# Optimization experiments

Measured on AMD Instinct MI355X. Metric: run time of the kernel, lower is better.

The kernel has to match this reference:

```python
import jax, jax.numpy as jnp
import numpy as np

B, T, C, H, N = 4, 4096, 2048, 32, 64
DMIX, DDEC = 32, 64
N_LAYER, LAYER_ID = 24, 12
GN_EPS = 1e-5 * 8.0 ** 2  # eps = 1e-5 * head_size_divisor**2


def setup_inputs() -> dict:
    key = jax.random.key(0)
    ks = jax.random.split(key, 24)
    r01 = LAYER_ID / (N_LAYER - 1)
    r1a0 = 1.0 - LAYER_ID / N_LAYER
    ddd = (np.arange(C, dtype=np.float32) / C).reshape(1, 1, C)
    maa = lambda p: jnp.asarray(1.0 - ddd ** p, dtype=jnp.float32)
    # decay speed schedule (canonical RWKV6, over channel dim)
    n = np.arange(C, dtype=np.float32)
    decay = (-6.0 + 5.0 * (n / (C - 1)) ** (0.7 + 1.3 * r01)).reshape(1, 1, C)
    # time_faaaa zigzag schedule
    m = np.arange(C, dtype=np.float32)
    zig = ((m + 1) % 3 - 1) * 0.1
    faaaa = (r01 * (1 - m / (C - 1)) + zig).reshape(H, N)
    s = 1.0 / np.sqrt(C)
    return {
        "x": jax.random.normal(ks[0], (B, T, C), jnp.float32),
        "shift_state": jax.random.normal(ks[1], (B, C), jnp.float32),
        "wkv_state": jnp.zeros((B, H, N, N), jnp.float32),
        "time_maa_x": maa(r1a0),
        "time_maa_w": maa(r1a0),
        "time_maa_k": maa(r1a0),
        "time_maa_v": jnp.asarray(1.0 - (ddd ** r1a0 + 0.3 * r01), jnp.float32),
        "time_maa_r": maa(0.5 * r1a0),
        "time_maa_g": maa(0.5 * r1a0),
        "time_maa_w1": jax.random.normal(ks[2], (C, 5 * DMIX), jnp.float32) * 0.01,
        "time_maa_w2": jax.random.uniform(ks[3], (5, DMIX, C), jnp.float32, -0.01, 0.01),
        "time_decay": jnp.asarray(decay, jnp.float32),
        "time_decay_w1": jax.random.normal(ks[4], (C, DDEC), jnp.float32) * 0.01,
        "time_decay_w2": jax.random.uniform(ks[5], (DDEC, C), jnp.float32, -0.01, 0.01),
        "time_faaaa": jnp.asarray(faaaa, jnp.float32),
        "Wr": jax.random.normal(ks[6], (C, C), jnp.float32) * s,
        "Wk": jax.random.normal(ks[7], (C, C), jnp.float32) * s,
        "Wv": jax.random.normal(ks[8], (C, C), jnp.float32) * s,
        "Wg": jax.random.normal(ks[9], (C, C), jnp.float32) * s,
        "Wo": jax.random.normal(ks[10], (C, C), jnp.float32) * s,
        "gn_weight": jnp.ones((C,), jnp.float32),
        "gn_bias": jnp.zeros((C,), jnp.float32),
    }


def reference(x, shift_state, wkv_state, time_maa_x, time_maa_w, time_maa_k,
              time_maa_v, time_maa_r, time_maa_g, time_maa_w1, time_maa_w2,
              time_decay, time_decay_w1, time_decay_w2, time_faaaa,
              Wr, Wk, Wv, Wg, Wo, gn_weight, gn_bias):
    b, t, c = x.shape
    # token shift: previous token (seeded by shift_state) minus current
    xx = jnp.concatenate([shift_state[:, None, :], x[:, :-1]], axis=1) - x
    lx = x[:, -1]
    # LoRA token-shift mixing
    xxx = x + xx * time_maa_x
    t5 = jnp.tanh(xxx @ time_maa_w1).reshape(b, t, 5, DMIX)
    mixes = jnp.einsum('btfd,fdc->fbtc', t5, time_maa_w2)
    mw, mk, mv, mr, mg = mixes
    xw = x + xx * (time_maa_w + mw)
    xk = x + xx * (time_maa_k + mk)
    xv = x + xx * (time_maa_v + mv)
    xr = x + xx * (time_maa_r + mr)
    xg = x + xx * (time_maa_g + mg)
    r = xr @ Wr
    k = xk @ Wk
    v = xv @ Wv
    g = jax.nn.silu(xg @ Wg)
    # data-dependent decay via LoRA; wkv6 uses log-decay -exp(w)
    w = time_decay + jnp.tanh(xw @ time_decay_w1) @ time_decay_w2
    glog = -jnp.exp(w)  # [b,t,c]
    to_heads = lambda z: z.reshape(b, t, H, N).transpose(1, 0, 2, 3)  # [t,b,h,n]
    rh, kh, vh, gh = to_heads(r), to_heads(k), to_heads(v), to_heads(glog)
    u = time_faaaa  # [H,N]

    def step(S, inp):
        r_t, k_t, v_t, g_t = inp  # each [b,h,n]
        kv = jnp.einsum('bhk,bhv->bhkv', k_t, v_t)
        o_t = jnp.einsum('bhk,bhkv->bhv', r_t, S + u[None, :, :, None] * kv)
        S = jnp.exp(g_t)[..., None] * S + kv
        return S, o_t

    state, o = jax.lax.scan(step, wkv_state, (rh, kh, vh, gh))
    o = o.transpose(1, 0, 2, 3).reshape(b, t, c)  # [b,t,c]
    # GroupNorm with H groups over channel dim
    og = o.reshape(b, t, H, N)
    mu = og.mean(-1, keepdims=True)
    var = og.var(-1, keepdims=True)
    on = (og - mu) * jax.lax.rsqrt(var + GN_EPS)
    on = on * gn_weight.reshape(H, N) + gn_bias.reshape(H, N)
    out = (on.reshape(b, t, c) * g) @ Wo
    return out, lx, state
```

## Files before the change

### kernel.cpp

```cpp
#include <hip/hip_runtime.h>
#include <hip/hip_bf16.h>
#include <stdint.h>

#define DEV __device__ __forceinline__

typedef __bf16 bf16x8 __attribute__((ext_vector_type(8)));
typedef float f32x4 __attribute__((ext_vector_type(4)));
typedef unsigned short u16x8 __attribute__((ext_vector_type(8)));

constexpr int kB = 4, kT = 4096, kC = 2048, kH = 32, kN = 64;
constexpr int kM = kB * kT;
constexpr int SEGN = 8, TSEG = kT / SEGN, CHN = TSEG / 64;

DEV float bfu2f(unsigned short u) {
  union { uint32_t i; float f; } x; x.i = ((uint32_t)u) << 16; return x.f;
}
DEV unsigned short f2bfu(float f) {
  union { float f; uint32_t i; } x; x.f = f;
  uint32_t r = x.i + 0x7FFFu + ((x.i >> 16) & 1u);
  return (unsigned short)(r >> 16);
}

DEV void gld16(const void* g, void* l) {
  __builtin_amdgcn_global_load_lds(
      (const __attribute__((address_space(1))) void*)g,
      (__attribute__((address_space(3))) void*)l, 16, 0, 0);
}

DEV int swzb(int row, int byteoff) { return (row << 7) + (byteoff ^ ((row & 7) << 4)); }

__global__ __launch_bounds__(256) void trans_bf16(
    const float* __restrict__ in, unsigned short* __restrict__ out, int R, int Cn) {
  __shared__ __attribute__((aligned(16))) unsigned short tile[64][65];
  const int t = threadIdx.x;
  const int r0 = blockIdx.y * 64, c0 = blockIdx.x * 64;
  const int lr = t >> 6, lc = t & 63;
#pragma unroll
  for (int i = 0; i < 16; i++) {
    int rr = lr + i * 4;
    int gr = r0 + rr, gc = c0 + lc;
    if (gr < R && gc < Cn) tile[rr][lc] = f2bfu(in[(size_t)gr * Cn + gc]);
  }
  __syncthreads();
#pragma unroll
  for (int i = 0; i < 16; i++) {
    int cc = lr + i * 4;
    int gc = c0 + cc, gr = r0 + lc;
    if (gc < Cn && gr < R) out[(size_t)gc * R + gr] = tile[lc][cc];
  }
}

__global__ __launch_bounds__(256) void prep_x2(
    const float* __restrict__ x, const float* __restrict__ shift,
    const float* __restrict__ maax,
    unsigned short* __restrict__ xxx, float* __restrict__ lx) {
  size_t i4 = ((size_t)blockIdx.x * 256 + threadIdx.x) * 4;
  int c = (int)(i4 & (kC - 1));
  size_t bt = i4 >> 11;
  int tt = (int)(bt & (kT - 1));
  int b = (int)(bt >> 12);
  float4 xv = *(const float4*)(x + i4);
  float4 pv = (tt == 0) ? *(const float4*)(shift + (size_t)b * kC + c)
                        : *(const float4*)(x + i4 - kC);
  float4 mx = *(const float4*)(maax + c);
  ushort4 o4;
  o4.x = f2bfu(xv.x + (pv.x - xv.x) * mx.x);
  o4.y = f2bfu(xv.y + (pv.y - xv.y) * mx.y);
  o4.z = f2bfu(xv.z + (pv.z - xv.z) * mx.z);
  o4.w = f2bfu(xv.w + (pv.w - xv.w) * mx.w);
  *(ushort4*)(xxx + i4) = o4;
  if (tt == kT - 1) *(float4*)(lx + (size_t)b * kC + c) = xv;
}

enum { E_F32 = 0, E_BF16 = 1, E_TANH = 2, E_SILU = 3, E_DECAY = 4 };

template <int BM, int BN, int EPI>
__global__ __launch_bounds__(256) void gemm_k(
    const unsigned short* __restrict__ A, const unsigned short* __restrict__ Bt,
    void* __restrict__ Cout, const float* __restrict__ aux, int M, int N, int K) {
  constexpr int WGM = (BM == 128 && BN == 128) ? 2 : (BM == 64 ? 2 : 4);
  constexpr int WGN = 4 / WGM;
  constexpr int WM = BM / WGM, WN = BN / WGN;
  constexpr int WR = WM / 16, WC = WN / 16;
  __shared__ __attribute__((aligned(16))) unsigned short As[BM * 32];
  __shared__ __attribute__((aligned(16))) unsigned short Bs[BN * 32];
  const int t = threadIdx.x, wid = t >> 6, l = t & 63;
  const int m0 = blockIdx.x * BM, n0 = blockIdx.y * BN;
  const int wm0 = (wid / WGN) * WM, wn0 = (wid % WGN) * WN;
  f32x4 acc[WR][WC];
#pragma unroll
  for (int i = 0; i < WR; i++)
#pragma unroll
    for (int j = 0; j < WC; j++) acc[i][j] = f32x4{0.f, 0.f, 0.f, 0.f};

  const int rowS = t >> 2, cbS = (t & 3) * 16;
  const char* Ab = (const char*)A;
  const char* Bb = (const char*)Bt;
  const int aoff = (wm0 + (l & 15)) * 32 + (l >> 4) * 8;
  const int boff = (wn0 + (l & 15)) * 32 + (l >> 4) * 8;

  for (int kt = 0; kt < K; kt += 32) {
#pragma unroll
    for (int ia = 0; ia < BM / 64; ia++)
      gld16(Ab + ((size_t)(m0 + ia * 64 + rowS) * K + kt) * 2 + cbS,
            (char*)As + ia * 4096 + wid * 1024);
    if constexpr (BN >= 64) {
#pragma unroll
      for (int ib = 0; ib < BN / 64; ib++)
        gld16(Bb + ((size_t)(n0 + ib * 64 + rowS) * K + kt) * 2 + cbS,
              (char*)Bs + ib * 4096 + wid * 1024);
    } else {
      if (t < BN * 4)
        gld16(Bb + ((size_t)(n0 + rowS) * K + kt) * 2 + cbS,
              (char*)Bs + wid * 1024);
    }
    __syncthreads();
    bf16x8 af[WR], bfv[WC];
#pragma unroll
    for (int mi = 0; mi < WR; mi++) af[mi] = *(const bf16x8*)(&As[aoff + mi * 512]);
#pragma unroll
    for (int ni = 0; ni < WC; ni++) bfv[ni] = *(const bf16x8*)(&Bs[boff + ni * 512]);
#pragma unroll
    for (int mi = 0; mi < WR; mi++)
#pragma unroll
      for (int ni = 0; ni < WC; ni++)
        acc[mi][ni] = __builtin_amdgcn_mfma_f32_16x16x32_bf16(af[mi], bfv[ni], acc[mi][ni], 0, 0, 0);
    __syncthreads();
  }

#pragma unroll
  for (int mi = 0; mi < WR; mi++) {
#pragma unroll
    for (int ni = 0; ni < WC; ni++) {
      int row = m0 + wm0 + mi * 16 + (l >> 4) * 4;
      int col = n0 + wn0 + ni * 16 + (l & 15);
#pragma unroll
      for (int j = 0; j < 4; j++) {
        float v = acc[mi][ni][j];
        size_t idx = (size_t)(row + j) * N + col;
        if constexpr (EPI == E_F32) ((float*)Cout)[idx] = v;
        else if constexpr (EPI == E_BF16) ((unsigned short*)Cout)[idx] = f2bfu(v);
        else if constexpr (EPI == E_TANH) ((unsigned short*)Cout)[idx] = f2bfu(tanhf(v));
        else if constexpr (EPI == E_SILU) ((unsigned short*)Cout)[idx] = f2bfu(v / (1.f + expf(-v)));
        else if constexpr (EPI == E_DECAY) {
          float w = v + aux[col];
          ((float*)Cout)[idx] = expf(-expf(w));
        }
      }
    }
  }
}

template <int EPI>
__global__ __launch_bounds__(512, 2) void gemm256_k(
    const unsigned short* __restrict__ A, const unsigned short* __restrict__ Bt,
    void* __restrict__ Cout, int M, int N, int K) {
  extern __shared__ __attribute__((aligned(16))) char lds[];
  const int tid = threadIdx.x, wid = tid >> 6, l = tid & 63;

  const int mtiles = M >> 8, ntiles = N >> 8;
  const int slab = mtiles >> 3;
  const int xcd = blockIdx.x & 7, loc = blockIdx.x >> 3;
  const int m0 = (xcd * slab + loc / ntiles) * 256;
  const int n0 = (loc % ntiles) * 256;

  const int wm = (wid >> 2) * 128, wn = (wid & 3) * 64;

  const int srow = tid >> 3;
  const int scb = (tid & 7) * 16;
  const char* pa[4]; const char* pb[4];
#pragma unroll
  for (int i = 0; i < 4; i++) {
    int row = i * 64 + srow;
    int cb = scb ^ ((row & 7) << 4);
    pa[i] = (const char*)A + (size_t)(m0 + row) * K * 2 + cb;
    pb[i] = (const char*)Bt + (size_t)(n0 + row) * K * 2 + cb;
  }

  int aof[2][2][8], bof[2][2][4];
#pragma unroll
  for (int bu = 0; bu < 2; bu++)
#pragma unroll
    for (int ks = 0; ks < 2; ks++) {
#pragma unroll
      for (int mi = 0; mi < 8; mi++)
        aof[bu][ks][mi] = bu * 65536 + swzb(wm + mi * 16 + (l & 15), ks * 64 + (l >> 4) * 16);
#pragma unroll
      for (int ni = 0; ni < 4; ni++)
        bof[bu][ks][ni] = bu * 65536 + 32768 + swzb(wn + ni * 16 + (l & 15), ks * 64 + (l >> 4) * 16);
    }

  f32x4 acc[8][4];
#pragma unroll
  for (int i = 0; i < 8; i++)
#pragma unroll
    for (int j = 0; j < 4; j++) acc[i][j] = f32x4{0.f, 0.f, 0.f, 0.f};

  auto STAGE = [&](int bu, int tb) {
#pragma unroll
    for (int i = 0; i < 4; i++) {
      gld16(pa[i] + tb, lds + bu * 65536 + i * 8192 + wid * 1024);
      gld16(pb[i] + tb, lds + bu * 65536 + 32768 + i * 8192 + wid * 1024);
    }
  };
  auto COMPUTE = [&](int bu) {
    __builtin_amdgcn_s_setprio(1);
#pragma unroll
    for (int ks = 0; ks < 2; ks++) {
      bf16x8 a[8];
#pragma unroll
      for (int mi = 0; mi < 8; mi++) a[mi] = *(const bf16x8*)(lds + aof[bu][ks][mi]);
#pragma unroll
      for (int ni = 0; ni < 4; ni++) {
        bf16x8 b = *(const bf16x8*)(lds + bof[bu][ks][ni]);
#pragma unroll
        for (int mi = 0; mi < 8; mi++)
          acc[mi][ni] = __builtin_amdgcn_mfma_f32_16x16x32_bf16(a[mi], b, acc[mi][ni], 0, 0, 0);
      }
    }
    __builtin_amdgcn_s_setprio(0);
  };

  const int KT = K >> 6;
  STAGE(0, 0);
  STAGE(1, 128);

  for (int t = 0; t + 3 < KT; t += 2) {
    asm volatile("s_waitcnt vmcnt(8)" ::: "memory");
    __builtin_amdgcn_s_barrier();
    __builtin_amdgcn_sched_barrier(0);
    COMPUTE(0);
    asm volatile("s_waitcnt lgkmcnt(0)" ::: "memory");
    __builtin_amdgcn_s_barrier();
    __builtin_amdgcn_sched_barrier(0);
    STAGE(0, (t + 2) * 128);

    asm volatile("s_waitcnt vmcnt(8)" ::: "memory");
    __builtin_amdgcn_s_barrier();
    __builtin_amdgcn_sched_barrier(0);
    COMPUTE(1);
    asm volatile("s_waitcnt lgkmcnt(0)" ::: "memory");
    __builtin_amdgcn_s_barrier();
    __builtin_amdgcn_sched_barrier(0);
    STAGE(1, (t + 3) * 128);
  }

  asm volatile("s_waitcnt vmcnt(8)" ::: "memory");
  __builtin_amdgcn_s_barrier();
  __builtin_amdgcn_sched_barrier(0);
  COMPUTE(0);
  asm volatile("s_waitcnt vmcnt(0)" ::: "memory");
  __builtin_amdgcn_s_barrier();
  __builtin_amdgcn_sched_barrier(0);
  COMPUTE(1);

#pragma unroll
  for (int mi = 0; mi < 8; mi++)
#pragma unroll
    for (int ni = 0; ni < 4; ni++) {
      int row = m0 + wm + mi * 16 + (l >> 4) * 4;
      int col = n0 + wn + ni * 16 + (l & 15);
#pragma unroll
      for (int j = 0; j < 4; j++) {
        float v = acc[mi][ni][j];
        size_t idx = (size_t)(row + j) * N + col;
        if constexpr (EPI == E_F32) ((float*)Cout)[idx] = v;
        else if constexpr (EPI == E_BF16) ((unsigned short*)Cout)[idx] = f2bfu(v);
        else if constexpr (EPI == E_SILU) ((unsigned short*)Cout)[idx] = f2bfu(v / (1.f + expf(-v)));
      }
    }
}

__global__ __launch_bounds__(256) void mix2f_k(
    const unsigned short* __restrict__ t5, const unsigned short* __restrict__ w2t,
    const float* __restrict__ x, const float* __restrict__ shift,
    const float* __restrict__ maa1, const float* __restrict__ maa2,
    unsigned short* __restrict__ xo1, unsigned short* __restrict__ xo2,
    int f1, int f2) {
  __shared__ __attribute__((aligned(16))) unsigned short As1[64 * 32];
  __shared__ __attribute__((aligned(16))) unsigned short Bs1[64 * 32];
  __shared__ __attribute__((aligned(16))) unsigned short As2[64 * 32];
  __shared__ __attribute__((aligned(16))) unsigned short Bs2[64 * 32];
  const int t = threadIdx.x, wid = t >> 6, l = t & 63;
  const int m0 = blockIdx.x * 64, n0 = blockIdx.y * 64;
  const int wm0 = (wid >> 1) * 32, wn0 = (wid & 1) * 32;
  const int rowS = t >> 2, cbS = (t & 3) * 16;
  const int aoff = (wm0 + (l & 15)) * 32 + (l >> 4) * 8;
  const int boff = (wn0 + (l & 15)) * 32 + (l >> 4) * 8;

  gld16((const char*)t5 + ((size_t)(m0 + rowS) * 160 + f1 * 32) * 2 + cbS, (char*)As1 + wid * 1024);
  gld16((const char*)w2t + ((size_t)(n0 + rowS) * 160 + f1 * 32) * 2 + cbS, (char*)Bs1 + wid * 1024);
  gld16((const char*)t5 + ((size_t)(m0 + rowS) * 160 + f2 * 32) * 2 + cbS, (char*)As2 + wid * 1024);
  gld16((const char*)w2t + ((size_t)(n0 + rowS) * 160 + f2 * 32) * 2 + cbS, (char*)Bs2 + wid * 1024);
  __syncthreads();
  bf16x8 a10 = *(const bf16x8*)(&As1[aoff]), a11 = *(const bf16x8*)(&As1[aoff + 512]);
  bf16x8 b10 = *(const bf16x8*)(&Bs1[boff]), b11 = *(const bf16x8*)(&Bs1[boff + 512]);
  bf16x8 a20 = *(const bf16x8*)(&As2[aoff]), a21 = *(const bf16x8*)(&As2[aoff + 512]);
  bf16x8 b20 = *(const bf16x8*)(&Bs2[boff]), b21 = *(const bf16x8*)(&Bs2[boff + 512]);
  f32x4 ac1[2][2], ac2[2][2];
#pragma unroll
  for (int i = 0; i < 2; i++)
#pragma unroll
    for (int j = 0; j < 2; j++) { ac1[i][j] = f32x4{0.f, 0.f, 0.f, 0.f}; ac2[i][j] = f32x4{0.f, 0.f, 0.f, 0.f}; }
  ac1[0][0] = __builtin_amdgcn_mfma_f32_16x16x32_bf16(a10, b10, ac1[0][0], 0, 0, 0);
  ac1[0][1] = __builtin_amdgcn_mfma_f32_16x16x32_bf16(a10, b11, ac1[0][1], 0, 0, 0);
  ac1[1][0] = __builtin_amdgcn_mfma_f32_16x16x32_bf16(a11, b10, ac1[1][0], 0, 0, 0);
  ac1[1][1] = __builtin_amdgcn_mfma_f32_16x16x32_bf16(a11, b11, ac1[1][1], 0, 0, 0);
  ac2[0][0] = __builtin_amdgcn_mfma_f32_16x16x32_bf16(a20, b20, ac2[0][0], 0, 0, 0);
  ac2[0][1] = __builtin_amdgcn_mfma_f32_16x16x32_bf16(a20, b21, ac2[0][1], 0, 0, 0);
  ac2[1][0] = __builtin_amdgcn_mfma_f32_16x16x32_bf16(a21, b20, ac2[1][0], 0, 0, 0);
  ac2[1][1] = __builtin_amdgcn_mfma_f32_16x16x32_bf16(a21, b21, ac2[1][1], 0, 0, 0);

#pragma unroll
  for (int mi = 0; mi < 2; mi++)
#pragma unroll
    for (int ni = 0; ni < 2; ni++) {
      int row = m0 + wm0 + mi * 16 + (l >> 4) * 4;
      int col = n0 + wn0 + ni * 16 + (l & 15);
      float mv1 = maa1[col], mv2 = maa2[col];
#pragma unroll
      for (int j = 0; j < 4; j++) {
        int rrow = row + j;
        int tt = rrow & (kT - 1);
        size_t idx = (size_t)rrow * kC + col;
        float xv = x[idx];
        float pv = (tt == 0) ? shift[(size_t)(rrow >> 12) * kC + col] : x[idx - kC];
        float d = pv - xv;
        xo1[idx] = f2bfu(xv + d * (mv1 + ac1[mi][ni][j]));
        xo2[idx] = f2bfu(xv + d * (mv2 + ac2[mi][ni][j]));
      }
    }
}

__global__ __launch_bounds__(256) void mixf_k(
    const unsigned short* __restrict__ t5, const unsigned short* __restrict__ w2t,
    const float* __restrict__ x, const float* __restrict__ shift,
    const float* __restrict__ maa, unsigned short* __restrict__ xout, int f) {
  __shared__ __attribute__((aligned(16))) unsigned short As[64 * 32];
  __shared__ __attribute__((aligned(16))) unsigned short Bs[64 * 32];
  const int t = threadIdx.x, wid = t >> 6, l = t & 63;
  const int m0 = blockIdx.x * 64, n0 = blockIdx.y * 64;
  const int wm0 = (wid >> 1) * 32, wn0 = (wid & 1) * 32;
  const int rowS = t >> 2, cbS = (t & 3) * 16;
  const int aoff = (wm0 + (l & 15)) * 32 + (l >> 4) * 8;
  const int boff = (wn0 + (l & 15)) * 32 + (l >> 4) * 8;

  gld16((const char*)t5 + ((size_t)(m0 + rowS) * 160 + f * 32) * 2 + cbS, (char*)As + wid * 1024);
  gld16((const char*)w2t + ((size_t)(n0 + rowS) * 160 + f * 32) * 2 + cbS, (char*)Bs + wid * 1024);
  __syncthreads();
  bf16x8 a0 = *(const bf16x8*)(&As[aoff]), a1 = *(const bf16x8*)(&As[aoff + 512]);
  bf16x8 b0 = *(const bf16x8*)(&Bs[boff]), b1 = *(const bf16x8*)(&Bs[boff + 512]);
  f32x4 acc[2][2];
  acc[0][0] = f32x4{0.f, 0.f, 0.f, 0.f}; acc[0][1] = f32x4{0.f, 0.f, 0.f, 0.f};
  acc[1][0] = f32x4{0.f, 0.f, 0.f, 0.f}; acc[1][1] = f32x4{0.f, 0.f, 0.f, 0.f};
  acc[0][0] = __builtin_amdgcn_mfma_f32_16x16x32_bf16(a0, b0, acc[0][0], 0, 0, 0);
  acc[0][1] = __builtin_amdgcn_mfma_f32_16x16x32_bf16(a0, b1, acc[0][1], 0, 0, 0);
  acc[1][0] = __builtin_amdgcn_mfma_f32_16x16x32_bf16(a1, b0, acc[1][0], 0, 0, 0);
  acc[1][1] = __builtin_amdgcn_mfma_f32_16x16x32_bf16(a1, b1, acc[1][1], 0, 0, 0);

#pragma unroll
  for (int mi = 0; mi < 2; mi++)
#pragma unroll
    for (int ni = 0; ni < 2; ni++) {
      int row = m0 + wm0 + mi * 16 + (l >> 4) * 4;
      int col = n0 + wn0 + ni * 16 + (l & 15);
      float mv = maa[col];
#pragma unroll
      for (int j = 0; j < 4; j++) {
        int rrow = row + j;
        int tt = rrow & (kT - 1);
        size_t idx = (size_t)rrow * kC + col;
        float xv = x[idx];
        float pv = (tt == 0) ? shift[(size_t)(rrow >> 12) * kC + col] : x[idx - kC];
        xout[idx] = f2bfu(xv + (pv - xv) * (mv + acc[mi][ni][j]));
      }
    }
}

__global__ __launch_bounds__(256) void wkv_local_k(
    const unsigned short* __restrict__ kb, const unsigned short* __restrict__ vb,
    const float* __restrict__ ed, float* __restrict__ Lbuf, float* __restrict__ Dseg) {
  const int bid = blockIdx.x;
  const int bh = bid >> 3, seg = bid & 7;
  const int h = bh & 31, b = bh >> 5;
  const int tid = threadIdx.x, w = tid >> 6, l = tid & 63;
  __shared__ __attribute__((aligned(16))) unsigned short KQks[4096];
  __shared__ __attribute__((aligned(16))) unsigned short Vt[4096];
  __shared__ float segp[4][64];
  __shared__ float DLs[64];

  const int fr = l & 15, fq = l >> 4;
  f32x4 Sreg[4];
#pragma unroll
  for (int ni = 0; ni < 4; ni++) Sreg[ni] = f32x4{0.f, 0.f, 0.f, 0.f};

  float dtot = 1.f;
  float kv[16], dv[16], vv[16];
  {
    size_t g = ((size_t)b * kT + seg * TSEG + w * 16) * kC + h * 64 + l;
#pragma unroll
    for (int i = 0; i < 16; i++) {
      kv[i] = bfu2f(kb[g]); vv[i] = bfu2f(vb[g]); dv[i] = ed[g];
      g += kC;
    }
  }

  for (int ch = 0; ch < CHN; ++ch) {
    float p = 1.f;
#pragma unroll
    for (int i = 0; i < 16; i++) p *= dv[i];
    segp[w][l] = p;
    __syncthreads();
    float pre = 1.f;
    if (w > 0) pre *= segp[0][l];
    if (w > 1) pre *= segp[1][l];
    if (w > 2) pre *= segp[2][l];
    if (w == 3) DLs[l] = pre * p;

    unsigned short kqrow[16], vtrow[16];
    float run = pre;
#pragma unroll
    for (int i = 0; i < 16; i++) {
      run *= dv[i];
      kqrow[i] = f2bfu(kv[i] / run);
      vtrow[i] = f2bfu(vv[i]);
    }
    {
      u16x8 q0, q1, v0, v1;
#pragma unroll
      for (int j = 0; j < 8; j++) { q0[j] = kqrow[j]; q1[j] = kqrow[j + 8]; v0[j] = vtrow[j]; v1[j] = vtrow[j + 8]; }
      *(u16x8*)((char*)KQks + swzb(l, w * 32)) = q0;
      *(u16x8*)((char*)KQks + swzb(l, w * 32 + 16)) = q1;
      *(u16x8*)((char*)Vt + swzb(l, w * 32)) = v0;
      *(u16x8*)((char*)Vt + swzb(l, w * 32 + 16)) = v1;
    }
    if (ch < CHN - 1) {
      size_t g = ((size_t)b * kT + seg * TSEG + (ch + 1) * 64 + w * 16) * kC + h * 64 + l;
#pragma unroll
      for (int i = 0; i < 16; i++) {
        kv[i] = bfu2f(kb[g]); vv[i] = bfu2f(vb[g]); dv[i] = ed[g];
        g += kC;
      }
    }
    __syncthreads();

    bf16x8 kA0 = *(const bf16x8*)((const char*)KQks + swzb(w * 16 + fr, fq * 16));
    bf16x8 kA1 = *(const bf16x8*)((const char*)KQks + swzb(w * 16 + fr, fq * 16 + 64));
    f32x4 kvacc[4];
#pragma unroll
    for (int ni = 0; ni < 4; ni++) {
      bf16x8 bv0 = *(const bf16x8*)((const char*)Vt + swzb(ni * 16 + fr, fq * 16));
      bf16x8 bv1 = *(const bf16x8*)((const char*)Vt + swzb(ni * 16 + fr, fq * 16 + 64));
      kvacc[ni] = __builtin_amdgcn_mfma_f32_16x16x32_bf16(kA0, bv0, f32x4{0.f, 0.f, 0.f, 0.f}, 0, 0, 0);
      kvacc[ni] = __builtin_amdgcn_mfma_f32_16x16x32_bf16(kA1, bv1, kvacc[ni], 0, 0, 0);
    }
    float dlj[4];
#pragma unroll
    for (int j = 0; j < 4; j++) dlj[j] = DLs[w * 16 + fq * 4 + j];
#pragma unroll
    for (int ni = 0; ni < 4; ni++)
#pragma unroll
      for (int j = 0; j < 4; j++)
        Sreg[ni][j] = (Sreg[ni][j] + kvacc[ni][j]) * dlj[j];
    dtot *= DLs[l];
    __syncthreads();
  }

  float* Lp = Lbuf + (size_t)bid * 4096;
#pragma unroll
  for (int ni = 0; ni < 4; ni++)
#pragma unroll
    for (int j = 0; j < 4; j++)
      Lp[(size_t)(w * 16 + fq * 4 + j) * 64 + ni * 16 + fr] = Sreg[ni][j];
  if (w == 0) Dseg[(size_t)bid * 64 + l] = dtot;
}

__global__ __launch_bounds__(256) void wkv_combine_k(
    const float* __restrict__ s0, const float* __restrict__ Dseg,
    float* __restrict__ Lbuf, float* __restrict__ sOut) {
  const int bh = blockIdx.x, tid = threadIdx.x;
  const int k = tid >> 2, v0 = (tid & 3) * 16;
  float4 s[4];
  const float* sp = s0 + (size_t)bh * 4096 + (size_t)k * 64 + v0;
#pragma unroll
  for (int q = 0; q < 4; q++) s[q] = ((const float4*)sp)[q];
  for (int seg = 0; seg < SEGN; ++seg) {
    size_t idx = (size_t)bh * SEGN + seg;
    float d = Dseg[idx * 64 + k];
    float* Lp = Lbuf + idx * 4096 + (size_t)k * 64 + v0;
#pragma unroll
    for (int q = 0; q < 4; q++) {
      float4 lq = ((float4*)Lp)[q];
      ((float4*)Lp)[q] = s[q];
      s[q].x = d * s[q].x + lq.x; s[q].y = d * s[q].y + lq.y;
      s[q].z = d * s[q].z + lq.z; s[q].w = d * s[q].w + lq.w;
    }
  }
  float* op = sOut + (size_t)bh * 4096 + (size_t)k * 64 + v0;
#pragma unroll
  for (int q = 0; q < 4; q++) ((float4*)op)[q] = s[q];
}

__global__ __launch_bounds__(256) void wkv_seg_k(
    const unsigned short* __restrict__ rb, const unsigned short* __restrict__ kb,
    const unsigned short* __restrict__ vb, const float* __restrict__ ed,
    const float* __restrict__ uf, const float* __restrict__ Sini,
    unsigned short* __restrict__ o) {
  const int bid = blockIdx.x;
  const int bh = bid >> 3, seg = bid & 7;
  const int h = bh & 31, b = bh >> 5;
  const int tid = threadIdx.x, w = tid >> 6, l = tid & 63;
  __shared__ __attribute__((aligned(16))) unsigned short RQ[4096];
  __shared__ __attribute__((aligned(16))) unsigned short KQsk[4096];
  __shared__ __attribute__((aligned(16))) unsigned short KQks[4096];
  __shared__ __attribute__((aligned(16))) unsigned short Vt[4096];
  __shared__ __attribute__((aligned(16))) unsigned short Pl[4096];
  __shared__ __attribute__((aligned(16))) unsigned short S0T[4096];
  __shared__ __attribute__((aligned(16))) unsigned short RU[4096];
  __shared__ __attribute__((aligned(16))) unsigned short Ksk[4096];
  __shared__ float segp[4][64];
  __shared__ float DLs[64];

  const float uu = uf[h * 64 + l];
  const int fr = l & 15, fq = l >> 4;

  f32x4 Sreg[4];
#pragma unroll
  for (int ni = 0; ni < 4; ni++)
#pragma unroll
    for (int j = 0; j < 4; j++) {
      int kk2 = w * 16 + fq * 4 + j, vv2 = ni * 16 + fr;
      float sv = Sini[(size_t)bid * 4096 + (size_t)kk2 * 64 + vv2];
      Sreg[ni][j] = sv;
      *(unsigned short*)((char*)S0T + swzb(vv2, kk2 * 2)) = f2bfu(sv);
    }
  __syncthreads();

  float rv[16], kv[16], dv[16], vv[16];
  {
    size_t g = ((size_t)b * kT + seg * TSEG + w * 16) * kC + h * 64 + l;
#pragma unroll
    for (int i = 0; i < 16; i++) {
      rv[i] = bfu2f(rb[g]); kv[i] = bfu2f(kb[g]); vv[i] = bfu2f(vb[g]); dv[i] = ed[g];
      g += kC;
    }
  }

  for (int ch = 0; ch < CHN; ++ch) {
    float p = 1.f;
#pragma unroll
    for (int i = 0; i < 16; i++) p *= dv[i];
    segp[w][l] = p;
    __syncthreads();
    float pre = 1.f;
    if (w > 0) pre *= segp[0][l];
    if (w > 1) pre *= segp[1][l];
    if (w > 2) pre *= segp[2][l];
    if (w == 3) DLs[l] = pre * p;

    unsigned short kqrow[16], vtrow[16];
    float run = pre;
#pragma unroll
    for (int i = 0; i < 16; i++) {
      int t = w * 16 + i;
      float rq = rv[i] * run;
      run *= dv[i];
      float kq = kv[i] / run;
      *(unsigned short*)((char*)RQ + swzb(t, l * 2)) = f2bfu(rq);
      *(unsigned short*)((char*)RU + swzb(t, l * 2)) = f2bfu(rv[i] * uu);
      *(unsigned short*)((char*)Ksk + swzb(t, l * 2)) = f2bfu(kv[i]);
      unsigned short kqu = f2bfu(kq);
      *(unsigned short*)((char*)KQsk + swzb(t, l * 2)) = kqu;
      kqrow[i] = kqu;
      vtrow[i] = f2bfu(vv[i]);
    }
    {
      u16x8 q0, q1, v0, v1;
#pragma unroll
      for (int j = 0; j < 8; j++) { q0[j] = kqrow[j]; q1[j] = kqrow[j + 8]; v0[j] = vtrow[j]; v1[j] = vtrow[j + 8]; }
      *(u16x8*)((char*)KQks + swzb(l, w * 32)) = q0;
      *(u16x8*)((char*)KQks + swzb(l, w * 32 + 16)) = q1;
      *(u16x8*)((char*)Vt + swzb(l, w * 32)) = v0;
      *(u16x8*)((char*)Vt + swzb(l, w * 32 + 16)) = v1;
    }

    if (ch < CHN - 1) {
      size_t g = ((size_t)b * kT + seg * TSEG + (ch + 1) * 64 + w * 16) * kC + h * 64 + l;
#pragma unroll
      for (int i = 0; i < 16; i++) {
        rv[i] = bfu2f(rb[g]); kv[i] = bfu2f(kb[g]); vv[i] = bfu2f(vb[g]); dv[i] = ed[g];
        g += kC;
      }
    }
    __syncthreads();

    bf16x8 a0 = *(const bf16x8*)((const char*)RQ + swzb(w * 16 + fr, fq * 16));
    bf16x8 a1 = *(const bf16x8*)((const char*)RQ + swzb(w * 16 + fr, fq * 16 + 64));
    f32x4 pacc[4];
#pragma unroll
    for (int ni = 0; ni < 4; ni++) {
      bf16x8 b0 = *(const bf16x8*)((const char*)KQsk + swzb(ni * 16 + fr, fq * 16));
      bf16x8 b1 = *(const bf16x8*)((const char*)KQsk + swzb(ni * 16 + fr, fq * 16 + 64));
      pacc[ni] = __builtin_amdgcn_mfma_f32_16x16x32_bf16(a0, b0, f32x4{0.f, 0.f, 0.f, 0.f}, 0, 0, 0);
      pacc[ni] = __builtin_amdgcn_mfma_f32_16x16x32_bf16(a1, b1, pacc[ni], 0, 0, 0);
    }
    f32x4 dacc;
    {
      bf16x8 ru0 = *(const bf16x8*)((const char*)RU + swzb(w * 16 + fr, fq * 16));
      bf16x8 ru1 = *(const bf16x8*)((const char*)RU + swzb(w * 16 + fr, fq * 16 + 64));
      bf16x8 kb0 = *(const bf16x8*)((const char*)Ksk + swzb(w * 16 + fr, fq * 16));
      bf16x8 kb1 = *(const bf16x8*)((const char*)Ksk + swzb(w * 16 + fr, fq * 16 + 64));
      dacc = __builtin_amdgcn_mfma_f32_16x16x32_bf16(ru0, kb0, f32x4{0.f, 0.f, 0.f, 0.f}, 0, 0, 0);
      dacc = __builtin_amdgcn_mfma_f32_16x16x32_bf16(ru1, kb1, dacc, 0, 0, 0);
    }
    float dg[4];
#pragma unroll
    for (int j = 0; j < 4; j++) dg[j] = __shfl(dacc[j], fq * 20 + j, 64);
#pragma unroll
    for (int ni = 0; ni < 4; ni++)
#pragma unroll
      for (int j = 0; j < 4; j++) {
        int row = w * 16 + fq * 4 + j, col = ni * 16 + fr;
        float pv = pacc[ni][j];
        pv = (col < row) ? pv : ((col == row) ? dg[j] : 0.f);
        *(unsigned short*)((char*)Pl + swzb(row, col * 2)) = f2bfu(pv);
      }
    __syncthreads();

    bf16x8 pA0 = *(const bf16x8*)((const char*)Pl + swzb(w * 16 + fr, fq * 16));
    bf16x8 pA1 = *(const bf16x8*)((const char*)Pl + swzb(w * 16 + fr, fq * 16 + 64));
    bf16x8 kA0 = *(const bf16x8*)((const char*)KQks + swzb(w * 16 + fr, fq * 16));
    bf16x8 kA1 = *(const bf16x8*)((const char*)KQks + swzb(w * 16 + fr, fq * 16 + 64));
    f32x4 oacc[4], kvacc[4];
#pragma unroll
    for (int ni = 0; ni < 4; ni++) {
      bf16x8 bv0 = *(const bf16x8*)((const char*)Vt + swzb(ni * 16 + fr, fq * 16));
      bf16x8 bv1 = *(const bf16x8*)((const char*)Vt + swzb(ni * 16 + fr, fq * 16 + 64));
      bf16x8 bs0 = *(const bf16x8*)((const char*)S0T + swzb(ni * 16 + fr, fq * 16));
      bf16x8 bs1 = *(const bf16x8*)((const char*)S0T + swzb(ni * 16 + fr, fq * 16 + 64));
      oacc[ni] = __builtin_amdgcn_mfma_f32_16x16x32_bf16(pA0, bv0, f32x4{0.f, 0.f, 0.f, 0.f}, 0, 0, 0);
      oacc[ni] = __builtin_amdgcn_mfma_f32_16x16x32_bf16(pA1, bv1, oacc[ni], 0, 0, 0);
      oacc[ni] = __builtin_amdgcn_mfma_f32_16x16x32_bf16(a0, bs0, oacc[ni], 0, 0, 0);
      oacc[ni] = __builtin_amdgcn_mfma_f32_16x16x32_bf16(a1, bs1, oacc[ni], 0, 0, 0);
      kvacc[ni] = __builtin_amdgcn_mfma_f32_16x16x32_bf16(kA0, bv0, f32x4{0.f, 0.f, 0.f, 0.f}, 0, 0, 0);
      kvacc[ni] = __builtin_amdgcn_mfma_f32_16x16x32_bf16(kA1, bv1, kvacc[ni], 0, 0, 0);
    }
    size_t obase = ((size_t)b * kT + seg * TSEG + ch * 64) * kC + h * 64;
#pragma unroll
    for (int ni = 0; ni < 4; ni++)
#pragma unroll
      for (int j = 0; j < 4; j++)
        o[obase + (size_t)(w * 16 + fq * 4 + j) * kC + ni * 16 + fr] = f2bfu(oacc[ni][j]);
    __syncthreads();

    float dlj[4];
#pragma unroll
    for (int j = 0; j < 4; j++) dlj[j] = DLs[w * 16 + fq * 4 + j];
#pragma unroll
    for (int ni = 0; ni < 4; ni++)
#pragma unroll
      for (int j = 0; j < 4; j++) {
        int kk2 = w * 16 + fq * 4 + j, vv2 = ni * 16 + fr;
        float sn = (Sreg[ni][j] + kvacc[ni][j]) * dlj[j];
        Sreg[ni][j] = sn;
        *(unsigned short*)((char*)S0T + swzb(vv2, kk2 * 2)) = f2bfu(sn);
      }
    __syncthreads();
  }
}

__global__ __launch_bounds__(256) void gn_k(
    const unsigned short* __restrict__ o, const unsigned short* __restrict__ gb,
    const float* __restrict__ gnw, const float* __restrict__ gnb,
    unsigned short* __restrict__ y) {
  int gi = blockIdx.x * 4 + (threadIdx.x >> 6);
  int j = threadIdx.x & 63;
  int bt = gi >> 5, h = gi & 31;
  size_t idx = (size_t)bt * kC + h * 64 + j;
  float val = bfu2f(o[idx]);
  float s = val, s2 = val * val;
#pragma unroll
  for (int m = 1; m < 64; m <<= 1) {
    s += __shfl_xor(s, m, 64);
    s2 += __shfl_xor(s2, m, 64);
  }
  float mu = s * 0.015625f;
  float var = s2 * 0.015625f - mu * mu;
  float rs = rsqrtf(var + 6.4e-4f);
  float on = (val - mu) * rs * gnw[h * 64 + j] + gnb[h * 64 + j];
  y[idx] = f2bfu(on * bfu2f(gb[idx]));
}

constexpr size_t SZW     = (size_t)2048 * 2048 * 2;
constexpr size_t OFF_WRT = 0;
constexpr size_t OFF_WKT = 1 * SZW;
constexpr size_t OFF_WVT = 2 * SZW;
constexpr size_t OFF_WGT = 3 * SZW;
constexpr size_t OFF_WOT = 4 * SZW;
constexpr size_t OFF_W1T = 5 * SZW;
constexpr size_t OFF_W2T = OFF_W1T + (size_t)160 * 2048 * 2;
constexpr size_t OFF_TD1 = OFF_W2T + (size_t)2048 * 160 * 2;
constexpr size_t OFF_TD2 = OFF_TD1 + (size_t)64 * 2048 * 2;
constexpr size_t OFF_T5  = OFF_TD2 + (size_t)2048 * 64 * 2;
constexpr size_t OFF_DT  = OFF_T5 + (size_t)kM * 160 * 2;
constexpr size_t OFF_EDEC= OFF_DT + (size_t)kM * 64 * 2;
constexpr size_t OFF_XMIX= OFF_EDEC + (size_t)kM * kC * 4;
constexpr size_t OFF_R   = OFF_XMIX + (size_t)kM * kC * 2;
constexpr size_t OFF_K   = OFF_R + (size_t)kM * kC * 2;
constexpr size_t OFF_V   = OFF_K + (size_t)kM * kC * 2;
constexpr size_t OFF_L   = OFF_WRT;

extern "C" void kernel_launch(void* const* d_in, const int* in_sizes, int n_in,
                              void* d_out, int out_size, void* d_ws, size_t ws_size,
                              hipStream_t stream) {
  const float* x     = (const float*)d_in[0];
  const float* shift = (const float*)d_in[1];
  const float* s0    = (const float*)d_in[2];
  const float* maax  = (const float*)d_in[3];
  const float* maaw  = (const float*)d_in[4];
  const float* maak  = (const float*)d_in[5];
  const float* maav  = (const float*)d_in[6];
  const float* maar  = (const float*)d_in[7];
  const float* maag  = (const float*)d_in[8];
  const float* w1    = (const float*)d_in[9];
  const float* w2    = (const float*)d_in[10];
  const float* tdec  = (const float*)d_in[11];
  const float* tdw1  = (const float*)d_in[12];
  const float* tdw2  = (const float*)d_in[13];
  const float* faaaa = (const float*)d_in[14];
  const float* Wr    = (const float*)d_in[15];
  const float* Wk    = (const float*)d_in[16];
  const float* Wv    = (const float*)d_in[17];
  const float* Wg    = (const float*)d_in[18];
  const float* Wo    = (const float*)d_in[19];
  const float* gnw   = (const float*)d_in[20];
  const float* gnb   = (const float*)d_in[21];

  char* ws = (char*)d_ws;
  unsigned short* Wrt  = (unsigned short*)(ws + OFF_WRT);
  unsigned short* Wkt  = (unsigned short*)(ws + OFF_WKT);
  unsigned short* Wvt  = (unsigned short*)(ws + OFF_WVT);
  unsigned short* Wgt  = (unsigned short*)(ws + OFF_WGT);
  unsigned short* Wot  = (unsigned short*)(ws + OFF_WOT);
  unsigned short* w1t  = (unsigned short*)(ws + OFF_W1T);
  unsigned short* w2t  = (unsigned short*)(ws + OFF_W2T);
  unsigned short* td1t = (unsigned short*)(ws + OFF_TD1);
  unsigned short* td2t = (unsigned short*)(ws + OFF_TD2);
  unsigned short* t5   = (unsigned short*)(ws + OFF_T5);
  unsigned short* dtmp = (unsigned short*)(ws + OFF_DT);
  float*          edec = (float*)(ws + OFF_EDEC);
  unsigned short* xg   = (unsigned short*)(ws + OFF_EDEC);
  unsigned short* bufX = (unsigned short*)(ws + OFF_XMIX);
  unsigned short* bufR = (unsigned short*)(ws + OFF_R);
  unsigned short* bufK = (unsigned short*)(ws + OFF_K);
  unsigned short* bufV = (unsigned short*)(ws + OFF_V);
  float*          Lbuf = (float*)(ws + OFF_L);
  float*          DsegP= (float*)(ws + OFF_TD1);

  float* outp  = (float*)d_out;
  float* lx    = outp + (size_t)kM * kC;
  float* stOut = lx + (size_t)kB * kC;

  dim3 blk(256);

  trans_bf16<<<dim3(32, 32), blk, 0, stream>>>(Wr, Wrt, 2048, 2048);
  trans_bf16<<<dim3(32, 32), blk, 0, stream>>>(Wk, Wkt, 2048, 2048);
  trans_bf16<<<dim3(32, 32), blk, 0, stream>>>(Wv, Wvt, 2048, 2048);
  trans_bf16<<<dim3(32, 32), blk, 0, stream>>>(Wg, Wgt, 2048, 2048);
  trans_bf16<<<dim3(32, 32), blk, 0, stream>>>(Wo, Wot, 2048, 2048);
  trans_bf16<<<dim3(3, 32), blk, 0, stream>>>(w1, w1t, 2048, 160);
  trans_bf16<<<dim3(1, 32), blk, 0, stream>>>(tdw1, td1t, 2048, 64);
  trans_bf16<<<dim3(32, 1), blk, 0, stream>>>(tdw2, td2t, 64, 2048);
  trans_bf16<<<dim3(32, 3), blk, 0, stream>>>(w2, w2t, 160, 2048);

  prep_x2<<<dim3(kM * kC / 4 / 256), blk, 0, stream>>>(x, shift, maax, bufX, lx);

  gemm_k<128, 32, E_TANH><<<dim3(kM / 128, 5), blk, 0, stream>>>(bufX, w1t, t5, nullptr, kM, 160, 2048);

  dim3 mgrid(kM / 64, kC / 64);
  constexpr int G256 = (kM / 256) * (kC / 256);
  constexpr size_t LDS256 = 131072;

  mix2f_k<<<mgrid, blk, 0, stream>>>(t5, w2t, x, shift, maaw, maak, bufX, bufV, 0, 1);
  gemm_k<64, 64, E_TANH><<<dim3(kM / 64, 1), blk, 0, stream>>>(bufX, td1t, dtmp, nullptr, kM, 64, 2048);
  gemm_k<128, 128, E_DECAY><<<dim3(kM / 128, 16), blk, 0, stream>>>(dtmp, td2t, edec, tdec, kM, 2048, 64);
  gemm256_k<E_BF16><<<dim3(G256), dim3(512), LDS256, stream>>>(bufV, Wkt, bufK, kM, 2048, 2048);

  mix2f_k<<<mgrid, blk, 0, stream>>>(t5, w2t, x, shift, maav, maar, bufX, bufV, 2, 3);
  gemm256_k<E_BF16><<<dim3(G256), dim3(512), LDS256, stream>>>(bufX, Wvt, bufR, kM, 2048, 2048);
  gemm256_k<E_BF16><<<dim3(G256), dim3(512), LDS256, stream>>>(bufV, Wrt, bufX, kM, 2048, 2048);

  wkv_local_k<<<dim3(kB * kH * SEGN), blk, 0, stream>>>(bufK, bufR, edec, Lbuf, DsegP);
  wkv_combine_k<<<dim3(kB * kH), blk, 0, stream>>>(s0, DsegP, Lbuf, stOut);
  wkv_seg_k<<<dim3(kB * kH * SEGN), blk, 0, stream>>>(bufX, bufK, bufR, edec, faaaa, Lbuf, bufV);

  mixf_k<<<mgrid, blk, 0, stream>>>(t5, w2t, x, shift, maag, xg, 4);
  gemm256_k<E_SILU><<<dim3(G256), dim3(512), LDS256, stream>>>(xg, Wgt, bufK, kM, 2048, 2048);

  gn_k<<<dim3(kM * kH / 4), blk, 0, stream>>>(bufV, bufK, gnw, gnb, bufR);

  gemm256_k<E_F32><<<dim3(G256), dim3(512), LDS256, stream>>>(bufR, Wot, outp, kM, 2048, 2048);
}
```

Baseline: 1.544 ms.

## Restructure 256x256 GEMM pipeline into half-K phases with interleaved staging

The 256-tile GEMM main loop is reorganised. Each 64-wide K tile is split into two 32-wide sub-stages stored in 64-byte swizzled rows. Each phase loads its fragments from LDS, issues the global-to-LDS prefetch for the matching sub-stage of the next tile, then runs its MFMAs. This replaces the separate compute/wait/stage sequence with its extra lgkmcnt barrier, so global loads overlap with MFMA work more finely and fewer barriers wait on full LDS drains. The cost is more barriers per K tile and a new swizzle pattern that could bring LDS bank conflicts or ordering hazards.

```diff
diff --git a/kernel.cpp b/kernel.cpp
--- a/kernel.cpp
+++ b/kernel.cpp
@@ -28,6 +28,7 @@
 }
 
 DEV int swzb(int row, int byteoff) { return (row << 7) + (byteoff ^ ((row & 7) << 4)); }
+DEV int swz64(int row, int byteoff) { return (row << 6) + (byteoff ^ ((row & 3) << 4)); }
 
 __global__ __launch_bounds__(256) void trans_bf16(
     const float* __restrict__ in, unsigned short* __restrict__ out, int R, int Cn) {
@@ -157,6 +158,7 @@
     void* __restrict__ Cout, int M, int N, int K) {
   extern __shared__ __attribute__((aligned(16))) char lds[];
   const int tid = threadIdx.x, wid = tid >> 6, l = tid & 63;
+  const int fr = l & 15, fq = l >> 4;
 
   const int mtiles = M >> 8, ntiles = N >> 8;
   const int slab = mtiles >> 3;
@@ -166,100 +168,83 @@
 
   const int wm = (wid >> 2) * 128, wn = (wid & 3) * 64;
 
-  const int srow = tid >> 3;
-  const int scb = (tid & 7) * 16;
-  const char* pa[4]; const char* pb[4];
-#pragma unroll
-  for (int i = 0; i < 4; i++) {
-    int row = i * 64 + srow;
-    int cb = scb ^ ((row & 7) << 4);
-    pa[i] = (const char*)A + (size_t)(m0 + row) * K * 2 + cb;
-    pb[i] = (const char*)Bt + (size_t)(n0 + row) * K * 2 + cb;
-  }
-
-  int aof[2][2][8], bof[2][2][4];
-#pragma unroll
-  for (int bu = 0; bu < 2; bu++)
-#pragma unroll
-    for (int ks = 0; ks < 2; ks++) {
+  const int srow0 = tid >> 2;
+  const int scb = ((tid & 3) * 16) ^ ((srow0 & 3) << 4);
+  const char* pa2[2]; const char* pb2[2];
+#pragma unroll
+  for (int i = 0; i < 2; i++) {
+    pa2[i] = (const char*)A + (size_t)(m0 + i * 128 + srow0) * K * 2 + scb;
+    pb2[i] = (const char*)Bt + (size_t)(n0 + i * 128 + srow0) * K * 2 + scb;
+  }
+
+  const char* vA[8]; const char* vB[4];
+#pragma unroll
+  for (int mi = 0; mi < 8; mi++)
+    vA[mi] = lds + swz64(wm + mi * 16 + fr, fq * 16);
+#pragma unroll
+  for (int ni = 0; ni < 4; ni++)
+    vB[ni] = lds + 32768 + swz64(wn + ni * 16 + fr, fq * 16);
+
+  f32x4 acc[8][4];
+#pragma unroll
+  for (int i = 0; i < 8; i++)
+#pragma unroll
+    for (int j = 0; j < 4; j++) acc[i][j] = f32x4{0.f, 0.f, 0.f, 0.f};
+
+  auto STG = [&](int q, int s, int ktb) {
+    const int d = q * 65536 + s * 16384 + wid * 1024;
+    gld16(pa2[0] + ktb + s * 64, lds + d);
+    gld16(pa2[1] + ktb + s * 64, lds + d + 8192);
+    gld16(pb2[0] + ktb + s * 64, lds + 32768 + d);
+    gld16(pb2[1] + ktb + s * 64, lds + 32768 + d + 8192);
+  };
+
+  auto PH = [&](int p, int s, bool doStage, int ktbNext, int vm) {
+    if (vm)
+      asm volatile("s_waitcnt vmcnt(4)" ::: "memory");
+    else
+      asm volatile("s_waitcnt vmcnt(0)" ::: "memory");
+    __builtin_amdgcn_s_barrier();
+    __builtin_amdgcn_sched_barrier(0);
+    const int pb = p * 65536 + s * 16384;
+    bf16x8 a[8], b[4];
+#pragma unroll
+    for (int mi = 0; mi < 8; mi++) a[mi] = *(const bf16x8*)(vA[mi] + pb);
+#pragma unroll
+    for (int ni = 0; ni < 4; ni++) b[ni] = *(const bf16x8*)(vB[ni] + pb);
+    if (doStage) STG(p ^ 1, s, ktbNext);
+    __builtin_amdgcn_sched_barrier(0);
+    __builtin_amdgcn_s_setprio(1);
+#pragma unroll
+    for (int ni = 0; ni < 4; ni++)
 #pragma unroll
       for (int mi = 0; mi < 8; mi++)
-        aof[bu][ks][mi] = bu * 65536 + swzb(wm + mi * 16 + (l & 15), ks * 64 + (l >> 4) * 16);
-#pragma unroll
-      for (int ni = 0; ni < 4; ni++)
-        bof[bu][ks][ni] = bu * 65536 + 32768 + swzb(wn + ni * 16 + (l & 15), ks * 64 + (l >> 4) * 16);
-    }
-
-  f32x4 acc[8][4];
-#pragma unroll
-  for (int i = 0; i < 8; i++)
-#pragma unroll
-    for (int j = 0; j < 4; j++) acc[i][j] = f32x4{0.f, 0.f, 0.f, 0.f};
-
-  auto STAGE = [&](int bu, int tb) {
-#pragma unroll
-    for (int i = 0; i < 4; i++) {
-      gld16(pa[i] + tb, lds + bu * 65536 + i * 8192 + wid * 1024);
-      gld16(pb[i] + tb, lds + bu * 65536 + 32768 + i * 8192 + wid * 1024);
-    }
-  };
-  auto COMPUTE = [&](int bu) {
-    __builtin_amdgcn_s_setprio(1);
-#pragma unroll
-    for (int ks = 0; ks < 2; ks++) {
-      bf16x8 a[8];
-#pragma unroll
-      for (int mi = 0; mi < 8; mi++) a[mi] = *(const bf16x8*)(lds + aof[bu][ks][mi]);
-#pragma unroll
-      for (int ni = 0; ni < 4; ni++) {
-        bf16x8 b = *(const bf16x8*)(lds + bof[bu][ks][ni]);
-#pragma unroll
-        for (int mi = 0; mi < 8; mi++)
-          acc[mi][ni] = __builtin_amdgcn_mfma_f32_16x16x32_bf16(a[mi], b, acc[mi][ni], 0, 0, 0);
-      }
-    }
+        acc[mi][ni] = __builtin_amdgcn_mfma_f32_16x16x32_bf16(a[mi], b[ni], acc[mi][ni], 0, 0, 0);
     __builtin_amdgcn_s_setprio(0);
   };
 
   const int KT = K >> 6;
-  STAGE(0, 0);
-  STAGE(1, 128);
-
-  for (int t = 0; t + 3 < KT; t += 2) {
-    asm volatile("s_waitcnt vmcnt(8)" ::: "memory");
-    __builtin_amdgcn_s_barrier();
-    __builtin_amdgcn_sched_barrier(0);
-    COMPUTE(0);
-    asm volatile("s_waitcnt lgkmcnt(0)" ::: "memory");
-    __builtin_amdgcn_s_barrier();
-    __builtin_amdgcn_sched_barrier(0);
-    STAGE(0, (t + 2) * 128);
-
-    asm volatile("s_waitcnt vmcnt(8)" ::: "memory");
-    __builtin_amdgcn_s_barrier();
-    __builtin_amdgcn_sched_barrier(0);
-    COMPUTE(1);
-    asm volatile("s_waitcnt lgkmcnt(0)" ::: "memory");
-    __builtin_amdgcn_s_barrier();
-    __builtin_amdgcn_sched_barrier(0);
-    STAGE(1, (t + 3) * 128);
-  }
-
-  asm volatile("s_waitcnt vmcnt(8)" ::: "memory");
-  __builtin_amdgcn_s_barrier();
-  __builtin_amdgcn_sched_barrier(0);
-  COMPUTE(0);
-  asm volatile("s_waitcnt vmcnt(0)" ::: "memory");
-  __builtin_amdgcn_s_barrier();
-  __builtin_amdgcn_sched_barrier(0);
-  COMPUTE(1);
+  STG(0, 0, 0);
+  STG(0, 1, 0);
+
+  int T = 0;
+  for (; T + 2 < KT; T += 2) {
+    PH(0, 0, true, (T + 1) * 128, 4);
+    PH(0, 1, true, (T + 1) * 128, 4);
+    PH(1, 0, true, (T + 2) * 128, 4);
+    PH(1, 1, true, (T + 2) * 128, 4);
+  }
+  PH(0, 0, true, (KT - 1) * 128, 4);
+  PH(0, 1, true, (KT - 1) * 128, 4);
+  PH(1, 0, false, 0, 4);
+  PH(1, 1, false, 0, 0);
 
 #pragma unroll
   for (int mi = 0; mi < 8; mi++)
 #pragma unroll
     for (int ni = 0; ni < 4; ni++) {
-      int row = m0 + wm + mi * 16 + (l >> 4) * 4;
-      int col = n0 + wn + ni * 16 + (l & 15);
+      int row = m0 + wm + mi * 16 + fq * 4;
+      int col = n0 + wn + ni * 16 + fr;
 #pragma unroll
       for (int j = 0; j < 4; j++) {
         float v = acc[mi][ni][j];
```

New measurement: 1.522 ms. About the same (-1.4%).
